# Optimization experiments

Measured on AMD Instinct MI355X. Metric: run time of the kernel, lower is better.

The kernel has to match this reference:

```python
import jax, jax.numpy as jnp
import numpy as np

IN, OUT, R, ALPHA = 4096, 4096, 32, 32
SCALE = ALPHA / R

def setup_inputs() -> dict:
    key = jax.random.key(0)
    k1, k2, k3, k4, k5 = jax.random.split(key, 5)
    x = jax.random.normal(k1, (4, 2048, IN), dtype=jnp.float32)
    weight = jax.random.normal(k2, (OUT, IN), dtype=jnp.float32) * 0.02
    bias = jax.random.normal(k3, (OUT,), dtype=jnp.float32) * 0.02
    A = jax.random.normal(k4, (OUT, R), dtype=jnp.float32) * 0.01
    # original init is zeros; use small randn so the LoRA path is nontrivial
    B = jax.random.normal(k5, (IN, R), dtype=jnp.float32) * 0.01
    return {"x": x, "weight": weight, "bias": bias, "A": A, "B": B}

def reference(x, weight, bias, A, B):
    # delta_w = A @ B.T * (alpha/r); y = x @ (W + delta_w).T + bias
    delta_w = (A @ B.T) * SCALE            # [out, in]
    w_eff = weight + delta_w
    return jnp.einsum('bsi,oi->bso', x, w_eff) + bias
```

## Files before the change

### kernel.cpp

```cpp
#include <hip/hip_runtime.h>

#define IN_DIM 4096
#define OUT_DIM 4096
#define M_DIM 8192
#define RANK 32
#define BK 64
#define NT (IN_DIM / BK)

typedef __bf16 bf16x8 __attribute__((ext_vector_type(8)));
typedef float f32x4 __attribute__((ext_vector_type(4)));

__device__ __forceinline__ unsigned short f2bf(float f) {
  unsigned u = __builtin_bit_cast(unsigned, f);
  u += 0x7FFF + ((u >> 16) & 1);
  return (unsigned short)(u >> 16);
}

__global__ __launch_bounds__(256) void prep_kernel(
    const float* __restrict__ X, unsigned short* __restrict__ Xb,
    const float* __restrict__ W, const float* __restrict__ A,
    const float* __restrict__ B, unsigned short* __restrict__ Wb) {
  const int tid = threadIdx.x;
  if (blockIdx.x >= 1024) {
    const int idx0 = (blockIdx.x - 1024) * 256 + tid;
    const int stride = 512 * 256;
    const int total4 = (M_DIM * IN_DIM) / 4;
    for (int i = idx0; i < total4; i += stride) {
      const float4 v = reinterpret_cast<const float4*>(X)[i];
      ushort4 o;
      o.x = f2bf(v.x); o.y = f2bf(v.y); o.z = f2bf(v.z); o.w = f2bf(v.w);
      reinterpret_cast<ushort4*>(Xb)[i] = o;
    }
    return;
  }
  __shared__ unsigned short sA[128][40];
  __shared__ unsigned short sB[128][40];
  const int lane = tid & 63;
  const int wid  = tid >> 6;
  const int wr   = wid >> 1, wc = wid & 1;
  const int li   = lane & 15, kg = lane >> 4;
  const int bRow = (blockIdx.x >> 5) * 128;
  const int bCol = (blockIdx.x & 31) * 128;

  for (int i = tid; i < 128 * 8; i += 256) {
    const int r = i >> 3, q = i & 7;
    const float4 va = reinterpret_cast<const float4*>(A + (size_t)(bRow + r) * RANK)[q];
    ushort4 oa;
    oa.x = f2bf(va.x); oa.y = f2bf(va.y); oa.z = f2bf(va.z); oa.w = f2bf(va.w);
    *reinterpret_cast<ushort4*>(&sA[r][q * 4]) = oa;
    const float4 vb = reinterpret_cast<const float4*>(B + (size_t)(bCol + r) * RANK)[q];
    ushort4 ob;
    ob.x = f2bf(vb.x); ob.y = f2bf(vb.y); ob.z = f2bf(vb.z); ob.w = f2bf(vb.w);
    *reinterpret_cast<ushort4*>(&sB[r][q * 4]) = ob;
  }
  __syncthreads();

  bf16x8 af[4], bq[4];
#pragma unroll
  for (int m = 0; m < 4; ++m)
    af[m] = *reinterpret_cast<const bf16x8*>(&sA[wr * 64 + m * 16 + li][kg * 8]);
#pragma unroll
  for (int n = 0; n < 4; ++n)
    bq[n] = *reinterpret_cast<const bf16x8*>(&sB[wc * 64 + n * 16 + li][kg * 8]);

  f32x4 acc[4][4];
#pragma unroll
  for (int m = 0; m < 4; ++m)
#pragma unroll
    for (int n = 0; n < 4; ++n) {
      acc[m][n] = f32x4{0.f, 0.f, 0.f, 0.f};
      acc[m][n] = __builtin_amdgcn_mfma_f32_16x16x32_bf16(af[m], bq[n], acc[m][n], 0, 0, 0);
    }

#pragma unroll
  for (int m = 0; m < 4; ++m) {
#pragma unroll
    for (int n = 0; n < 4; ++n) {
      const int col = bCol + wc * 64 + n * 16 + li;
#pragma unroll
      for (int j = 0; j < 4; ++j) {
        const int row = bRow + wr * 64 + m * 16 + kg * 4 + j;
        const size_t idx = (size_t)row * IN_DIM + col;
        Wb[idx] = f2bf(W[idx] + acc[m][n][j]);
      }
    }
  }
}

__global__ __launch_bounds__(512, 2) void gemm_kernel(
    const unsigned short* __restrict__ Xb, const unsigned short* __restrict__ Wb,
    const float* __restrict__ bias, float* __restrict__ Y) {
  __shared__ unsigned short lds[8][8192];
  const int tid  = threadIdx.x;
  const int lane = tid & 63;
  const int wid  = tid >> 6;
  const int wr   = wid >> 2;
  const int wc   = wid & 3;
  const int li   = lane & 15, kg = lane >> 4;

  const int bid = blockIdx.x;
  const int swz = (bid & 7) * 64 + (bid >> 3);
  const int bx  = swz & 15;
  const int by  = swz >> 4;
  const int bRow = by * 256, bCol = bx * 256;

  const int kcS = (tid & 7) ^ ((tid >> 3) & 7);
  const unsigned short* srcA[2][2];
  const unsigned short* srcB[2][2];
#pragma unroll
  for (int h = 0; h < 2; ++h)
#pragma unroll
    for (int l = 0; l < 2; ++l) {
      const int gA = l * 128 + h * 64 + (tid >> 3);
      const int gB = (l * 2 + (tid >> 8)) * 64 + h * 32 + ((tid >> 3) & 31);
      srcA[h][l] = Xb + (size_t)(bRow + gA) * IN_DIM + kcS * 8;
      srcB[h][l] = Wb + (size_t)(bCol + gB) * IN_DIM + kcS * 8;
    }
  char* const ldsRaw = (char*)&lds[0][0];

#define GLD(src, dstoff)                                                       \
  __builtin_amdgcn_global_load_lds(                                            \
      (const __attribute__((address_space(1))) unsigned int*)(src),            \
      (__attribute__((address_space(3))) unsigned int*)(ldsRaw + (dstoff)),    \
      16, 0, 0)
#define STAGE_A(s, h)                                                          \
  do {                                                                         \
    const int q_ = (((s) & 1) << 2) + (h);                                     \
    GLD(srcA[h][0] + (s) * BK, q_ * 16384 + tid * 16);                         \
    GLD(srcA[h][1] + (s) * BK, q_ * 16384 + 8192 + tid * 16);                  \
  } while (0)
#define STAGE_B(s, h)                                                          \
  do {                                                                         \
    const int q_ = (((s) & 1) << 2) + 2 + (h);                                 \
    GLD(srcB[h][0] + (s) * BK, q_ * 16384 + tid * 16);                         \
    GLD(srcB[h][1] + (s) * BK, q_ * 16384 + 8192 + tid * 16);                  \
  } while (0)
#define BAR() __builtin_amdgcn_s_barrier()

  const int rowAoff = (wr * 64 + li) * 64;
  const int rowBoff = (wc * 32 + li) * 64;
  int kx[2];
  kx[0] = ((0 * 4 + kg) ^ (li & 7)) * 8;
  kx[1] = ((1 * 4 + kg) ^ (li & 7)) * 8;

  bf16x8 af0[4], af1[4], bq0[4], bq1[4];
  f32x4 acc[8][4];
#pragma unroll
  for (int m = 0; m < 8; ++m)
#pragma unroll
    for (int n = 0; n < 4; ++n) acc[m][n] = f32x4{0.f, 0.f, 0.f, 0.f};

#define RD_AF(dst, dsel, h, ks)                                                \
  do {                                                                         \
    const unsigned short* a_ = &lds[((dsel) << 2) + (h)][0] + rowAoff;         \
    _Pragma("unroll") for (int mq = 0; mq < 4; ++mq)                           \
      dst[mq] = *reinterpret_cast<const bf16x8*>(a_ + mq * 1024 + kx[ks]);     \
  } while (0)
#define RD_BQ(dst, dsel, ks)                                                   \
  do {                                                                         \
    const unsigned short* b0_ = &lds[((dsel) << 2) + 2][0] + rowBoff;          \
    const unsigned short* b1_ = &lds[((dsel) << 2) + 3][0] + rowBoff;          \
    dst[0] = *reinterpret_cast<const bf16x8*>(b0_ + kx[ks]);                   \
    dst[1] = *reinterpret_cast<const bf16x8*>(b0_ + 1024 + kx[ks]);            \
    dst[2] = *reinterpret_cast<const bf16x8*>(b1_ + kx[ks]);                   \
    dst[3] = *reinterpret_cast<const bf16x8*>(b1_ + 1024 + kx[ks]);            \
  } while (0)
#define MM(base, afv, bqv)                                                     \
  do {                                                                         \
    __builtin_amdgcn_s_setprio(1);                                             \
    _Pragma("unroll") for (int mq = 0; mq < 4; ++mq)                           \
      _Pragma("unroll") for (int nq = 0; nq < 4; ++nq)                         \
        acc[(base) + mq][nq] = __builtin_amdgcn_mfma_f32_16x16x32_bf16(        \
            afv[mq], bqv[nq], acc[(base) + mq][nq], 0, 0, 0);                  \
    __builtin_amdgcn_s_setprio(0);                                             \
  } while (0)

  STAGE_A(0, 0); STAGE_B(0, 0); STAGE_A(0, 1); STAGE_B(0, 1);
  STAGE_A(1, 0); STAGE_B(1, 0);
  asm volatile("s_waitcnt vmcnt(4)" ::: "memory");
  BAR();
  RD_AF(af0, 0, 0, 0);
  RD_BQ(bq0, 0, 0);

  for (int t = 0; t < NT; ++t) {
    const int dcur = t & 1;
    const int dn   = dcur ^ 1;
    const bool st1 = (t + 1 < NT), st2 = (t + 2 < NT);
    if (st1) { STAGE_B(t + 1, 1); STAGE_A(t + 1, 1); }
    RD_AF(af1, dcur, 0, 1);
    RD_BQ(bq1, dcur, 1);
    BAR();
    MM(0, af0, bq0);
    RD_AF(af0, dcur, 1, 0);
    BAR();
    MM(0, af1, bq1);
    if (st2) STAGE_A(t + 2, 0);
    RD_AF(af1, dcur, 1, 1);
    if (st2) asm volatile("s_waitcnt vmcnt(2)" ::: "memory");
    else     asm volatile("s_waitcnt vmcnt(0)" ::: "memory");
    BAR();
    MM(4, af0, bq0);
    if (st2) STAGE_B(t + 2, 0);
    if (st1) { RD_AF(af0, dn, 0, 0); RD_BQ(bq0, dn, 0); }
    BAR();
    MM(4, af1, bq1);
  }
#undef GLD
#undef STAGE_A
#undef STAGE_B
#undef BAR
#undef RD_AF
#undef RD_BQ
#undef MM

#pragma unroll
  for (int nf = 0; nf < 4; ++nf) {
    const int col = bCol + wc * 64 + nf * 16 + li;
    const float bv = bias[col];
#pragma unroll
    for (int mf = 0; mf < 8; ++mf) {
      const int row0 = bRow + wr * 128 + mf * 16 + kg * 4;
#pragma unroll
      for (int j = 0; j < 4; ++j)
        Y[(size_t)(row0 + j) * OUT_DIM + col] = acc[mf][nf][j] + bv;
    }
  }
}

extern "C" void kernel_launch(void* const* d_in, const int* in_sizes, int n_in,
                              void* d_out, int out_size, void* d_ws, size_t ws_size,
                              hipStream_t stream) {
  const float* x    = (const float*)d_in[0];
  const float* w    = (const float*)d_in[1];
  const float* bias = (const float*)d_in[2];
  const float* A    = (const float*)d_in[3];
  const float* B    = (const float*)d_in[4];
  float* y = (float*)d_out;

  const size_t xb_bytes = (size_t)M_DIM * IN_DIM * 2;
  const size_t wb_bytes = (size_t)OUT_DIM * IN_DIM * 2;
  if (ws_size < xb_bytes + wb_bytes) return;

  unsigned short* Xb = (unsigned short*)d_ws;
  unsigned short* Wb = (unsigned short*)((char*)d_ws + xb_bytes);

  prep_kernel<<<1536, 256, 0, stream>>>(x, Xb, w, A, B, Wb);
  gemm_kernel<<<(M_DIM / 256) * (OUT_DIM / 256), 512, 0, stream>>>(Xb, Wb, bias, y);
}
```

Before: 280.3 us.

## Shrink GEMM tile to 128x256 with BK=32 and triple-buffered LDS pipeline

Replaces the 256x256 tile, BK=64 double-buffered, interleaved-read schedule with a 128x256 tile, BK=32, three-stage LDS ring that prefetches two steps ahead and uses one barrier per K step. Accumulators drop from 8x4 to 4x4 fragments and launch bounds move to 4 blocks per CU, aiming for more occupancy and more blocks to cover latency. In exchange, each block reuses less data per loaded byte, runs more K iterations each with less MFMA work, and loses the fine-grained read/compute interleaving of the old schedule.

```diff
diff --git a/kernel.cpp b/kernel.cpp
--- a/kernel.cpp
+++ b/kernel.cpp
@@ -4,7 +4,7 @@
 #define OUT_DIM 4096
 #define M_DIM 8192
 #define RANK 32
-#define BK 64
+#define BK 32
 #define NT (IN_DIM / BK)
 
 typedef __bf16 bf16x8 __attribute__((ext_vector_type(8)));
@@ -87,10 +87,10 @@
   }
 }
 
-__global__ __launch_bounds__(512, 2) void gemm_kernel(
+__global__ __launch_bounds__(512, 4) void gemm_kernel(
     const unsigned short* __restrict__ Xb, const unsigned short* __restrict__ Wb,
     const float* __restrict__ bias, float* __restrict__ Y) {
-  __shared__ unsigned short lds[8][8192];
+  __shared__ unsigned short lds[3 * 12288];
   const int tid  = threadIdx.x;
   const int lane = tid & 63;
   const int wid  = tid >> 6;
@@ -99,127 +99,84 @@
   const int li   = lane & 15, kg = lane >> 4;
 
   const int bid = blockIdx.x;
-  const int swz = (bid & 7) * 64 + (bid >> 3);
+  const int swz = (bid & 7) * 128 + (bid >> 3);
   const int bx  = swz & 15;
   const int by  = swz >> 4;
-  const int bRow = by * 256, bCol = bx * 256;
-
-  const int kcS = (tid & 7) ^ ((tid >> 3) & 7);
-  const unsigned short* srcA[2][2];
-  const unsigned short* srcB[2][2];
-#pragma unroll
-  for (int h = 0; h < 2; ++h)
-#pragma unroll
-    for (int l = 0; l < 2; ++l) {
-      const int gA = l * 128 + h * 64 + (tid >> 3);
-      const int gB = (l * 2 + (tid >> 8)) * 64 + h * 32 + ((tid >> 3) & 31);
-      srcA[h][l] = Xb + (size_t)(bRow + gA) * IN_DIM + kcS * 8;
-      srcB[h][l] = Wb + (size_t)(bCol + gB) * IN_DIM + kcS * 8;
-    }
-  char* const ldsRaw = (char*)&lds[0][0];
+  const int bRow = by * 128, bCol = bx * 256;
+
+  const int rS  = tid >> 2;
+  const int kcS = (tid & 3) ^ ((rS >> 1) & 3);
+  const unsigned short* srcA0 = Xb + (size_t)(bRow + rS) * IN_DIM + kcS * 8;
+  const unsigned short* srcB0 = Wb + (size_t)(bCol + rS) * IN_DIM + kcS * 8;
+  const unsigned short* srcB1 = srcB0 + (size_t)128 * IN_DIM;
+  char* const ldsRaw = (char*)&lds[0];
 
 #define GLD(src, dstoff)                                                       \
   __builtin_amdgcn_global_load_lds(                                            \
       (const __attribute__((address_space(1))) unsigned int*)(src),            \
       (__attribute__((address_space(3))) unsigned int*)(ldsRaw + (dstoff)),    \
       16, 0, 0)
-#define STAGE_A(s, h)                                                          \
+#define STAGE(s, base_)                                                        \
   do {                                                                         \
-    const int q_ = (((s) & 1) << 2) + (h);                                     \
-    GLD(srcA[h][0] + (s) * BK, q_ * 16384 + tid * 16);                         \
-    GLD(srcA[h][1] + (s) * BK, q_ * 16384 + 8192 + tid * 16);                  \
-  } while (0)
-#define STAGE_B(s, h)                                                          \
-  do {                                                                         \
-    const int q_ = (((s) & 1) << 2) + 2 + (h);                                 \
-    GLD(srcB[h][0] + (s) * BK, q_ * 16384 + tid * 16);                         \
-    GLD(srcB[h][1] + (s) * BK, q_ * 16384 + 8192 + tid * 16);                  \
+    GLD(srcA0 + (s) * BK, (base_) + tid * 16);                                 \
+    GLD(srcB0 + (s) * BK, (base_) + 8192 + tid * 16);                          \
+    GLD(srcB1 + (s) * BK, (base_) + 16384 + tid * 16);                         \
   } while (0)
 #define BAR() __builtin_amdgcn_s_barrier()
-
-  const int rowAoff = (wr * 64 + li) * 64;
-  const int rowBoff = (wc * 32 + li) * 64;
-  int kx[2];
-  kx[0] = ((0 * 4 + kg) ^ (li & 7)) * 8;
-  kx[1] = ((1 * 4 + kg) ^ (li & 7)) * 8;
-
-  bf16x8 af0[4], af1[4], bq0[4], bq1[4];
-  f32x4 acc[8][4];
-#pragma unroll
-  for (int m = 0; m < 8; ++m)
+#define VMCNT(n) __builtin_amdgcn_s_waitcnt(0x0F70 | (n))
+
+  const int kxs  = (kg ^ ((li >> 1) & 3)) * 8;
+  const int rdA  = (wr * 64 + li) * 32 + kxs;
+  const int rdB  = 4096 + (wc * 64 + li) * 32 + kxs;
+
+  bf16x8 af[4], bq[4];
+  f32x4 acc[4][4];
+#pragma unroll
+  for (int m = 0; m < 4; ++m)
 #pragma unroll
     for (int n = 0; n < 4; ++n) acc[m][n] = f32x4{0.f, 0.f, 0.f, 0.f};
 
-#define RD_AF(dst, dsel, h, ks)                                                \
-  do {                                                                         \
-    const unsigned short* a_ = &lds[((dsel) << 2) + (h)][0] + rowAoff;         \
-    _Pragma("unroll") for (int mq = 0; mq < 4; ++mq)                           \
-      dst[mq] = *reinterpret_cast<const bf16x8*>(a_ + mq * 1024 + kx[ks]);     \
-  } while (0)
-#define RD_BQ(dst, dsel, ks)                                                   \
-  do {                                                                         \
-    const unsigned short* b0_ = &lds[((dsel) << 2) + 2][0] + rowBoff;          \
-    const unsigned short* b1_ = &lds[((dsel) << 2) + 3][0] + rowBoff;          \
-    dst[0] = *reinterpret_cast<const bf16x8*>(b0_ + kx[ks]);                   \
-    dst[1] = *reinterpret_cast<const bf16x8*>(b0_ + 1024 + kx[ks]);            \
-    dst[2] = *reinterpret_cast<const bf16x8*>(b1_ + kx[ks]);                   \
-    dst[3] = *reinterpret_cast<const bf16x8*>(b1_ + 1024 + kx[ks]);            \
-  } while (0)
-#define MM(base, afv, bqv)                                                     \
-  do {                                                                         \
-    __builtin_amdgcn_s_setprio(1);                                             \
-    _Pragma("unroll") for (int mq = 0; mq < 4; ++mq)                           \
-      _Pragma("unroll") for (int nq = 0; nq < 4; ++nq)                         \
-        acc[(base) + mq][nq] = __builtin_amdgcn_mfma_f32_16x16x32_bf16(        \
-            afv[mq], bqv[nq], acc[(base) + mq][nq], 0, 0, 0);                  \
-    __builtin_amdgcn_s_setprio(0);                                             \
-  } while (0)
-
-  STAGE_A(0, 0); STAGE_B(0, 0); STAGE_A(0, 1); STAGE_B(0, 1);
-  STAGE_A(1, 0); STAGE_B(1, 0);
-  asm volatile("s_waitcnt vmcnt(4)" ::: "memory");
+  STAGE(0, 0);
+  STAGE(1, 24576);
+  VMCNT(3);
   BAR();
-  RD_AF(af0, 0, 0, 0);
-  RD_BQ(bq0, 0, 0);
-
+
+  int cur = 0;
   for (int t = 0; t < NT; ++t) {
-    const int dcur = t & 1;
-    const int dn   = dcur ^ 1;
-    const bool st1 = (t + 1 < NT), st2 = (t + 2 < NT);
-    if (st1) { STAGE_B(t + 1, 1); STAGE_A(t + 1, 1); }
-    RD_AF(af1, dcur, 0, 1);
-    RD_BQ(bq1, dcur, 1);
+    int nx = cur + 2; if (nx >= 3) nx -= 3;
+    const bool st2 = (t + 2 < NT);
+    if (st2) STAGE(t + 2, nx * 24576);
+    const unsigned short* base = &lds[cur * 12288];
+#pragma unroll
+    for (int mf = 0; mf < 4; ++mf)
+      af[mf] = *reinterpret_cast<const bf16x8*>(base + rdA + mf * 512);
+#pragma unroll
+    for (int nf = 0; nf < 4; ++nf)
+      bq[nf] = *reinterpret_cast<const bf16x8*>(base + rdB + nf * 512);
+    if (st2) VMCNT(3); else VMCNT(0);
     BAR();
-    MM(0, af0, bq0);
-    RD_AF(af0, dcur, 1, 0);
-    BAR();
-    MM(0, af1, bq1);
-    if (st2) STAGE_A(t + 2, 0);
-    RD_AF(af1, dcur, 1, 1);
-    if (st2) asm volatile("s_waitcnt vmcnt(2)" ::: "memory");
-    else     asm volatile("s_waitcnt vmcnt(0)" ::: "memory");
-    BAR();
-    MM(4, af0, bq0);
-    if (st2) STAGE_B(t + 2, 0);
-    if (st1) { RD_AF(af0, dn, 0, 0); RD_BQ(bq0, dn, 0); }
-    BAR();
-    MM(4, af1, bq1);
+    __builtin_amdgcn_s_setprio(1);
+#pragma unroll
+    for (int mf = 0; mf < 4; ++mf)
+#pragma unroll
+      for (int nf = 0; nf < 4; ++nf)
+        acc[mf][nf] = __builtin_amdgcn_mfma_f32_16x16x32_bf16(
+            af[mf], bq[nf], acc[mf][nf], 0, 0, 0);
+    __builtin_amdgcn_s_setprio(0);
+    if (++cur == 3) cur = 0;
   }
 #undef GLD
-#undef STAGE_A
-#undef STAGE_B
+#undef STAGE
 #undef BAR
-#undef RD_AF
-#undef RD_BQ
-#undef MM
+#undef VMCNT
 
 #pragma unroll
   for (int nf = 0; nf < 4; ++nf) {
     const int col = bCol + wc * 64 + nf * 16 + li;
     const float bv = bias[col];
 #pragma unroll
-    for (int mf = 0; mf < 8; ++mf) {
-      const int row0 = bRow + wr * 128 + mf * 16 + kg * 4;
+    for (int mf = 0; mf < 4; ++mf) {
+      const int row0 = bRow + wr * 64 + mf * 16 + kg * 4;
 #pragma unroll
       for (int j = 0; j < 4; ++j)
         Y[(size_t)(row0 + j) * OUT_DIM + col] = acc[mf][nf][j] + bv;
@@ -245,5 +202,5 @@
   unsigned short* Wb = (unsigned short*)((char*)d_ws + xb_bytes);
 
   prep_kernel<<<1536, 256, 0, stream>>>(x, Xb, w, A, B, Wb);
-  gemm_kernel<<<(M_DIM / 256) * (OUT_DIM / 256), 512, 0, stream>>>(Xb, Wb, bias, y);
-}
+  gemm_kernel<<<(M_DIM / 128) * (OUT_DIM / 256), 512, 0, stream>>>(Xb, Wb, bias, y);
+}
```

After: 341.4 us. 21.8% more time.
